# Kernel optimization log

Hardware: AMD Instinct MI355X
Metric: run time of the kernel (lower is better)

## Reference

```python
import jax, jax.numpy as jnp
import numpy as np

POOL = (2, 2)
B, H, W, C = 8, 128, 128, 256
FLAT_OUT = (H * POOL[0]) * (W * POOL[1]) * C  # 16,777,216


def setup_inputs() -> dict:
    key = jax.random.key(0)
    k1, k2 = jax.random.split(key)
    updates = jax.random.normal(k1, (B, H, W, C), dtype=jnp.float32)
    mask = jax.random.randint(k2, (B, H, W, C), 0, FLAT_OUT, dtype=jnp.int32)
    return {"updates": updates, "mask": mask}


def reference(updates, mask):
    ph, pw = POOL
    b, h, w, c = updates.shape
    hout, wout = h * ph, w * pw
    flat_input_size = h * w * c            # NOTE: original uses INPUT size as batch offset
    flat_output_size = hout * wout * c
    # per-batch offset (replicates b * flat_input_size from the TF code)
    batch_range = jnp.arange(b, dtype=jnp.int32).reshape(-1, 1, 1, 1)
    flat_mask = (mask.astype(jnp.int32) + batch_range * flat_input_size).reshape(-1)
    flat_updates = updates.reshape(-1)
    flat_output = jnp.zeros((b * flat_output_size,), dtype=updates.dtype)
    flat_output = flat_output.at[flat_mask].add(flat_updates)
    return flat_output.reshape(b, hout, wout, c)
```

## Files before the change

### kernel.cpp

```cpp
#include <hip/hip_runtime.h>


typedef float floatx4 __attribute__((ext_vector_type(4)));

constexpr int FLAT_IN   = 1 << 22;
constexpr int N_ELEMS   = 8 * FLAT_IN;
constexpr int OUT_WIN   = 7 * FLAT_IN + (1 << 24);
constexpr int OUT_TOTAL = 134217728;
constexpr int BKT_SHIFT = 14;
constexpr int BKT_SIZE  = 1 << BKT_SHIFT;
constexpr int NB        = OUT_WIN >> BKT_SHIFT;
constexpr int PBLOCK    = 1024;
constexpr int CHUNK     = 131072;
constexpr int NBLK      = N_ELEMS / CHUNK;
constexpr int ITERS     = CHUNK / (4 * PBLOCK);
constexpr int SEGS      = 8;
constexpr int SEG_ROWS  = NBLK / SEGS;

constexpr size_t WS_PAIRS  = 0;
constexpr size_t WS_HIST   = 268435456;
constexpr size_t WS_SEGSUM = WS_HIST + (size_t)NBLK * NB * 4;
constexpr size_t WS_BBASE  = WS_SEGSUM + (size_t)SEGS * NB * 4;
constexpr size_t WS_NEEDED = WS_BBASE + (size_t)(NB + 1) * 4;

__global__ __launch_bounds__(256) void zero_kernel(floatx4* __restrict__ p, int n4) {
  int i = blockIdx.x * 256 + threadIdx.x;
  int stride = gridDim.x * 256;
  floatx4 z = {0.f, 0.f, 0.f, 0.f};
  for (; i < n4; i += stride) __builtin_nontemporal_store(z, p + i);
}

__global__ __launch_bounds__(PBLOCK) void p1_hist(const int4* __restrict__ mask4,
                                                  int* __restrict__ hist) {
  __shared__ int cnt[NB];
  const int blk = blockIdx.x, tid = threadIdx.x;
  for (int j = tid; j < NB; j += PBLOCK) cnt[j] = 0;
  __syncthreads();
  const int base4 = blk * (CHUNK / 4);
  const int boff = (blk * CHUNK) & ~(FLAT_IN - 1);
  #pragma unroll 4
  for (int k = 0; k < ITERS; ++k) {
    int4 m = mask4[base4 + k * PBLOCK + tid];
    atomicAdd(&cnt[(m.x + boff) >> BKT_SHIFT], 1);
    atomicAdd(&cnt[(m.y + boff) >> BKT_SHIFT], 1);
    atomicAdd(&cnt[(m.z + boff) >> BKT_SHIFT], 1);
    atomicAdd(&cnt[(m.w + boff) >> BKT_SHIFT], 1);
  }
  __syncthreads();
  for (int j = tid; j < NB; j += PBLOCK) hist[blk * NB + j] = cnt[j];
}

__global__ __launch_bounds__(256) void p2_segsum(const int* __restrict__ hist,
                                                 int* __restrict__ segsum) {
  int b = blockIdx.x * 256 + threadIdx.x;
  int seg = blockIdx.y;
  const int* p = hist + (size_t)(seg * SEG_ROWS) * NB + b;
  int s = 0;
  #pragma unroll 4
  for (int k = 0; k < SEG_ROWS; ++k) s += p[(size_t)k * NB];
  segsum[seg * NB + b] = s;
}

__global__ __launch_bounds__(256) void p2_scan(const int* __restrict__ segsum,
                                               int* __restrict__ bbase) {
  __shared__ int tot[NB];
  __shared__ int partial[256];
  const int t = threadIdx.x;
  for (int j = t; j < NB; j += 256) {
    int s = 0;
    #pragma unroll
    for (int g = 0; g < SEGS; ++g) s += segsum[g * NB + j];
    tot[j] = s;
  }
  __syncthreads();
  int local = 0;
  #pragma unroll
  for (int k = 0; k < NB / 256; ++k) local += tot[t * (NB / 256) + k];
  partial[t] = local;
  __syncthreads();
  for (int off = 1; off < 256; off <<= 1) {
    int tmp = (t >= off) ? partial[t - off] : 0;
    __syncthreads();
    partial[t] += tmp;
    __syncthreads();
  }
  int run = partial[t] - local;
  #pragma unroll
  for (int k = 0; k < NB / 256; ++k) {
    int b = t * (NB / 256) + k;
    bbase[b] = run;
    run += tot[b];
  }
  if (t == 255) bbase[NB] = run;
}

__global__ __launch_bounds__(256) void p2_expand(int* __restrict__ hist,
                                                 const int* __restrict__ segsum) {
  int b = blockIdx.x * 256 + threadIdx.x;
  int seg = blockIdx.y;
  int run = 0;
  for (int g = 0; g < seg; ++g) run += segsum[g * NB + b];
  int* p = hist + (size_t)(seg * SEG_ROWS) * NB + b;
  for (int k = 0; k < SEG_ROWS; ++k) {
    int v = p[(size_t)k * NB];
    p[(size_t)k * NB] = run;
    run += v;
  }
}

__global__ __launch_bounds__(PBLOCK) void p3_place(const int4* __restrict__ mask4,
                                                   const float4* __restrict__ upd4,
                                                   const int* __restrict__ hist,
                                                   const int* __restrict__ bbase,
                                                   int2* __restrict__ pairs) {
  __shared__ int cnt[NB];
  __shared__ int rowbase[NB];
  const int blk = blockIdx.x, tid = threadIdx.x;
  for (int j = tid; j < NB; j += PBLOCK) {
    cnt[j] = 0;
    rowbase[j] = bbase[j] + hist[blk * NB + j];
  }
  __syncthreads();
  const int base4 = blk * (CHUNK / 4);
  const int boff = (blk * CHUNK) & ~(FLAT_IN - 1);
  #pragma unroll 2
  for (int k = 0; k < ITERS; ++k) {
    int j4 = base4 + k * PBLOCK + tid;
    int4 m = mask4[j4];
    float4 u = upd4[j4];
    {
      int idx = m.x + boff; int b = idx >> BKT_SHIFT;
      int r = atomicAdd(&cnt[b], 1);
      pairs[rowbase[b] + r] = make_int2(idx, __float_as_int(u.x));
    }
    {
      int idx = m.y + boff; int b = idx >> BKT_SHIFT;
      int r = atomicAdd(&cnt[b], 1);
      pairs[rowbase[b] + r] = make_int2(idx, __float_as_int(u.y));
    }
    {
      int idx = m.z + boff; int b = idx >> BKT_SHIFT;
      int r = atomicAdd(&cnt[b], 1);
      pairs[rowbase[b] + r] = make_int2(idx, __float_as_int(u.z));
    }
    {
      int idx = m.w + boff; int b = idx >> BKT_SHIFT;
      int r = atomicAdd(&cnt[b], 1);
      pairs[rowbase[b] + r] = make_int2(idx, __float_as_int(u.w));
    }
  }
}

__global__ __launch_bounds__(256) void p4_apply(const int2* __restrict__ pairs,
                                                const int* __restrict__ bbase,
                                                float* __restrict__ out) {
  __shared__ float win[BKT_SIZE];
  const int bkt = blockIdx.x, tid = threadIdx.x;
  floatx4* w4 = (floatx4*)win;
  floatx4 z = {0.f, 0.f, 0.f, 0.f};
  #pragma unroll
  for (int k = 0; k < BKT_SIZE / 1024; ++k) w4[k * 256 + tid] = z;
  __syncthreads();
  const int s = bbase[bkt], e = bbase[bkt + 1];
  const int s4 = (s + 1) & ~1;
  if ((s & 1) && s < e && tid == 0) {
    int2 p = pairs[s];
    atomicAdd(&win[p.x & (BKT_SIZE - 1)], __int_as_float(p.y));
  }
  const int n2 = (e > s4) ? ((e - s4) >> 1) : 0;
  const int4* pv = (const int4*)(pairs + s4);
  for (int i = tid; i < n2; i += 256) {
    int4 q = pv[i];
    atomicAdd(&win[q.x & (BKT_SIZE - 1)], __int_as_float(q.y));
    atomicAdd(&win[q.z & (BKT_SIZE - 1)], __int_as_float(q.w));
  }
  if ((e > s4) && ((e - s4) & 1) && tid == 0) {
    int2 p = pairs[e - 1];
    atomicAdd(&win[p.x & (BKT_SIZE - 1)], __int_as_float(p.y));
  }
  __syncthreads();
  floatx4* o4 = (floatx4*)(out + (size_t)bkt * BKT_SIZE);
  #pragma unroll
  for (int k = 0; k < BKT_SIZE / 1024; ++k)
    __builtin_nontemporal_store(w4[k * 256 + tid], o4 + k * 256 + tid);
}

__global__ __launch_bounds__(256) void scatter_add4_kernel(
    const float4* __restrict__ upd4, const int4* __restrict__ msk4,
    float* __restrict__ out, int n4) {
  int j = blockIdx.x * blockDim.x + threadIdx.x;
  if (j >= n4) return;
  float4 u = upd4[j];
  int4 m = msk4[j];
  int base = (j * 4) & ~(FLAT_IN - 1);
  unsafeAtomicAdd(out + (base + m.x), u.x);
  unsafeAtomicAdd(out + (base + m.y), u.y);
  unsafeAtomicAdd(out + (base + m.z), u.z);
  unsafeAtomicAdd(out + (base + m.w), u.w);
}

extern "C" void kernel_launch(void* const* d_in, const int* in_sizes, int n_in,
                              void* d_out, int out_size, void* d_ws, size_t ws_size,
                              hipStream_t stream) {
  const float* updates = (const float*)d_in[0];
  const int*   mask    = (const int*)d_in[1];
  float*       out     = (float*)d_out;
  const int n = in_sizes[0];

  const bool fast = (n == N_ELEMS) && (out_size == OUT_TOTAL) && (ws_size >= WS_NEEDED);

  if (!fast) {
    int n4z = out_size / 4;
    zero_kernel<<<(n4z + 2047) / 2048, 256, 0, stream>>>((floatx4*)d_out, n4z);
    int n4 = n / 4;
    scatter_add4_kernel<<<(n4 + 255) / 256, 256, 0, stream>>>(
        (const float4*)updates, (const int4*)mask, out, n4);
    return;
  }

  char* ws = (char*)d_ws;
  int2* pairs  = (int2*)(ws + WS_PAIRS);
  int*  hist   = (int*)(ws + WS_HIST);
  int*  segsum = (int*)(ws + WS_SEGSUM);
  int*  bbase  = (int*)(ws + WS_BBASE);

  {
    int n4 = (OUT_TOTAL - OUT_WIN) / 4;
    zero_kernel<<<5376, 256, 0, stream>>>((floatx4*)(out + OUT_WIN), n4);
  }
  p1_hist<<<NBLK, PBLOCK, 0, stream>>>((const int4*)mask, hist);
  p2_segsum<<<dim3(NB / 256, SEGS), 256, 0, stream>>>(hist, segsum);
  p2_scan<<<1, 256, 0, stream>>>(segsum, bbase);
  p2_expand<<<dim3(NB / 256, SEGS), 256, 0, stream>>>(hist, segsum);
  p3_place<<<NBLK, PBLOCK, 0, stream>>>((const int4*)mask, (const float4*)updates,
                                        hist, bbase, pairs);
  p4_apply<<<NB, 256, 0, stream>>>(pairs, bbase, out);
}
```

Before: 1.212 ms.

## Split bucket sort into coarse and fine passes with wave-aggregated fine placement

Replaces the single-pass bucket sort over 16K-element buckets with two passes. A coarse pass places pairs into 64K-element buckets using a small per-block shared histogram, with pairs staged in the unused tail of the output buffer. A fine pass then splits each coarse bucket into four fine buckets, using ballot-based wave aggregation to cut shared atomics. This is meant to shrink the per-block histogram and scan work and make the scattered pair writes more local, at the cost of an extra full read and write of the pair array.

```diff
diff --git a/kernel.cpp b/kernel.cpp
--- a/kernel.cpp
+++ b/kernel.cpp
@@ -7,21 +7,28 @@
 constexpr int N_ELEMS   = 8 * FLAT_IN;
 constexpr int OUT_WIN   = 7 * FLAT_IN + (1 << 24);
 constexpr int OUT_TOTAL = 134217728;
-constexpr int BKT_SHIFT = 14;
-constexpr int BKT_SIZE  = 1 << BKT_SHIFT;
-constexpr int NB        = OUT_WIN >> BKT_SHIFT;
-constexpr int PBLOCK    = 1024;
-constexpr int CHUNK     = 131072;
-constexpr int NBLK      = N_ELEMS / CHUNK;
-constexpr int ITERS     = CHUNK / (4 * PBLOCK);
-constexpr int SEGS      = 8;
-constexpr int SEG_ROWS  = NBLK / SEGS;
+
+constexpr int FB_SHIFT = 14;
+constexpr int BKT_SIZE = 1 << FB_SHIFT;
+constexpr int NBF      = OUT_WIN >> FB_SHIFT;
+constexpr int CB_SHIFT = 16;
+constexpr int NBC      = OUT_WIN >> CB_SHIFT;
+constexpr int NBC_PAD  = 768;
+
+constexpr int PBLOCK   = 1024;
+constexpr int CHUNK    = 131072;
+constexpr int NBLK     = N_ELEMS / CHUNK;
+constexpr int ITERS    = CHUNK / (4 * PBLOCK);
+constexpr int SEGS     = 8;
+constexpr int SEG_ROWS = NBLK / SEGS;
 
 constexpr size_t WS_PAIRS  = 0;
-constexpr size_t WS_HIST   = 268435456;
-constexpr size_t WS_SEGSUM = WS_HIST + (size_t)NBLK * NB * 4;
-constexpr size_t WS_BBASE  = WS_SEGSUM + (size_t)SEGS * NB * 4;
-constexpr size_t WS_NEEDED = WS_BBASE + (size_t)(NB + 1) * 4;
+constexpr size_t WS_HISTC  = 268435456;
+constexpr size_t WS_SEGC   = WS_HISTC + (size_t)NBLK * NBC_PAD * 4;
+constexpr size_t WS_BBC    = WS_SEGC + (size_t)SEGS * NBC_PAD * 4;
+constexpr size_t WS_FH     = WS_BBC + 3328;
+constexpr size_t WS_BBF    = WS_FH + (size_t)NBF * 4;
+constexpr size_t WS_NEEDED = WS_BBF + (size_t)(NBF + 1) * 4;
 
 __global__ __launch_bounds__(256) void zero_kernel(floatx4* __restrict__ p, int n4) {
   int i = blockIdx.x * 256 + threadIdx.x;
@@ -31,51 +38,62 @@
 }
 
 __global__ __launch_bounds__(PBLOCK) void p1_hist(const int4* __restrict__ mask4,
-                                                  int* __restrict__ hist) {
-  __shared__ int cnt[NB];
+                                                  int* __restrict__ hist_c,
+                                                  int* __restrict__ fhist) {
+  __shared__ int cnt[1024];
   const int blk = blockIdx.x, tid = threadIdx.x;
-  for (int j = tid; j < NB; j += PBLOCK) cnt[j] = 0;
+  if (tid < 1024) cnt[tid] = 0;
   __syncthreads();
   const int base4 = blk * (CHUNK / 4);
-  const int boff = (blk * CHUNK) & ~(FLAT_IN - 1);
   #pragma unroll 4
   for (int k = 0; k < ITERS; ++k) {
     int4 m = mask4[base4 + k * PBLOCK + tid];
-    atomicAdd(&cnt[(m.x + boff) >> BKT_SHIFT], 1);
-    atomicAdd(&cnt[(m.y + boff) >> BKT_SHIFT], 1);
-    atomicAdd(&cnt[(m.z + boff) >> BKT_SHIFT], 1);
-    atomicAdd(&cnt[(m.w + boff) >> BKT_SHIFT], 1);
-  }
-  __syncthreads();
-  for (int j = tid; j < NB; j += PBLOCK) hist[blk * NB + j] = cnt[j];
+    atomicAdd(&cnt[m.x >> FB_SHIFT], 1);
+    atomicAdd(&cnt[m.y >> FB_SHIFT], 1);
+    atomicAdd(&cnt[m.z >> FB_SHIFT], 1);
+    atomicAdd(&cnt[m.w >> FB_SHIFT], 1);
+  }
+  __syncthreads();
+  const int boff = (blk * CHUNK) & ~(FLAT_IN - 1);
+  const int f0   = boff >> FB_SHIFT;
+  const int cb0  = f0 >> 2;
+  for (int j = tid; j < 1024; j += PBLOCK)
+    if (cnt[j]) atomicAdd(&fhist[f0 + j], cnt[j]);
+  for (int j = tid; j < NBC_PAD; j += PBLOCK) {
+    int v = 0;
+    int jj = j - cb0;
+    if (jj >= 0 && jj < 256)
+      v = cnt[4 * jj] + cnt[4 * jj + 1] + cnt[4 * jj + 2] + cnt[4 * jj + 3];
+    hist_c[blk * NBC_PAD + j] = v;
+  }
 }
 
 __global__ __launch_bounds__(256) void p2_segsum(const int* __restrict__ hist,
                                                  int* __restrict__ segsum) {
   int b = blockIdx.x * 256 + threadIdx.x;
   int seg = blockIdx.y;
-  const int* p = hist + (size_t)(seg * SEG_ROWS) * NB + b;
+  const int* p = hist + (size_t)(seg * SEG_ROWS) * NBC_PAD + b;
   int s = 0;
   #pragma unroll 4
-  for (int k = 0; k < SEG_ROWS; ++k) s += p[(size_t)k * NB];
-  segsum[seg * NB + b] = s;
-}
-
-__global__ __launch_bounds__(256) void p2_scan(const int* __restrict__ segsum,
-                                               int* __restrict__ bbase) {
-  __shared__ int tot[NB];
+  for (int k = 0; k < SEG_ROWS; ++k) s += p[(size_t)k * NBC_PAD];
+  segsum[seg * NBC_PAD + b] = s;
+}
+
+__global__ __launch_bounds__(256) void p2_scan_c(const int* __restrict__ segsum,
+                                                 int* __restrict__ bbase) {
+  __shared__ int tot[NBC_PAD];
   __shared__ int partial[256];
   const int t = threadIdx.x;
-  for (int j = t; j < NB; j += 256) {
+  for (int j = t; j < NBC_PAD; j += 256) {
     int s = 0;
     #pragma unroll
-    for (int g = 0; g < SEGS; ++g) s += segsum[g * NB + j];
+    for (int g = 0; g < SEGS; ++g) s += segsum[g * NBC_PAD + j];
     tot[j] = s;
   }
   __syncthreads();
   int local = 0;
   #pragma unroll
-  for (int k = 0; k < NB / 256; ++k) local += tot[t * (NB / 256) + k];
+  for (int k = 0; k < NBC_PAD / 256; ++k) local += tot[t * (NBC_PAD / 256) + k];
   partial[t] = local;
   __syncthreads();
   for (int off = 1; off < 256; off <<= 1) {
@@ -86,12 +104,12 @@
   }
   int run = partial[t] - local;
   #pragma unroll
-  for (int k = 0; k < NB / 256; ++k) {
-    int b = t * (NB / 256) + k;
+  for (int k = 0; k < NBC_PAD / 256; ++k) {
+    int b = t * (NBC_PAD / 256) + k;
     bbase[b] = run;
     run += tot[b];
   }
-  if (t == 255) bbase[NB] = run;
+  if (t == 255) bbase[NBC_PAD] = run;
 }
 
 __global__ __launch_bounds__(256) void p2_expand(int* __restrict__ hist,
@@ -99,55 +117,131 @@
   int b = blockIdx.x * 256 + threadIdx.x;
   int seg = blockIdx.y;
   int run = 0;
-  for (int g = 0; g < seg; ++g) run += segsum[g * NB + b];
-  int* p = hist + (size_t)(seg * SEG_ROWS) * NB + b;
+  for (int g = 0; g < seg; ++g) run += segsum[g * NBC_PAD + b];
+  int* p = hist + (size_t)(seg * SEG_ROWS) * NBC_PAD + b;
   for (int k = 0; k < SEG_ROWS; ++k) {
-    int v = p[(size_t)k * NB];
-    p[(size_t)k * NB] = run;
+    int v = p[(size_t)k * NBC_PAD];
+    p[(size_t)k * NBC_PAD] = run;
     run += v;
   }
 }
 
-__global__ __launch_bounds__(PBLOCK) void p3_place(const int4* __restrict__ mask4,
-                                                   const float4* __restrict__ upd4,
-                                                   const int* __restrict__ hist,
-                                                   const int* __restrict__ bbase,
-                                                   int2* __restrict__ pairs) {
-  __shared__ int cnt[NB];
-  __shared__ int rowbase[NB];
+__global__ __launch_bounds__(256) void p2_scan_f(const int* __restrict__ fhist,
+                                                 int* __restrict__ bbase) {
+  __shared__ int tot[NBF];
+  __shared__ int partial[256];
+  const int t = threadIdx.x;
+  for (int j = t; j < NBF; j += 256) tot[j] = fhist[j];
+  __syncthreads();
+  int local = 0;
+  #pragma unroll
+  for (int k = 0; k < NBF / 256; ++k) local += tot[t * (NBF / 256) + k];
+  partial[t] = local;
+  __syncthreads();
+  for (int off = 1; off < 256; off <<= 1) {
+    int tmp = (t >= off) ? partial[t - off] : 0;
+    __syncthreads();
+    partial[t] += tmp;
+    __syncthreads();
+  }
+  int run = partial[t] - local;
+  #pragma unroll
+  for (int k = 0; k < NBF / 256; ++k) {
+    int b = t * (NBF / 256) + k;
+    bbase[b] = run;
+    run += tot[b];
+  }
+  if (t == 255) bbase[NBF] = run;
+}
+
+__global__ __launch_bounds__(PBLOCK) void p3a_place(const int4* __restrict__ mask4,
+                                                    const float4* __restrict__ upd4,
+                                                    const int* __restrict__ hist_c,
+                                                    const int* __restrict__ bbase_c,
+                                                    int2* __restrict__ pout) {
+  __shared__ int cnt[256];
+  __shared__ int rowbase[256];
   const int blk = blockIdx.x, tid = threadIdx.x;
-  for (int j = tid; j < NB; j += PBLOCK) {
-    cnt[j] = 0;
-    rowbase[j] = bbase[j] + hist[blk * NB + j];
+  const int boff = (blk * CHUNK) & ~(FLAT_IN - 1);
+  const int cb0 = boff >> CB_SHIFT;
+  if (tid < 256) {
+    cnt[tid] = 0;
+    rowbase[tid] = bbase_c[cb0 + tid] + hist_c[blk * NBC_PAD + cb0 + tid];
   }
   __syncthreads();
   const int base4 = blk * (CHUNK / 4);
-  const int boff = (blk * CHUNK) & ~(FLAT_IN - 1);
   #pragma unroll 2
   for (int k = 0; k < ITERS; ++k) {
     int j4 = base4 + k * PBLOCK + tid;
     int4 m = mask4[j4];
     float4 u = upd4[j4];
     {
-      int idx = m.x + boff; int b = idx >> BKT_SHIFT;
-      int r = atomicAdd(&cnt[b], 1);
-      pairs[rowbase[b] + r] = make_int2(idx, __float_as_int(u.x));
+      int b = m.x >> CB_SHIFT; int r = atomicAdd(&cnt[b], 1);
+      pout[rowbase[b] + r] = make_int2(m.x + boff, __float_as_int(u.x));
     }
     {
-      int idx = m.y + boff; int b = idx >> BKT_SHIFT;
-      int r = atomicAdd(&cnt[b], 1);
-      pairs[rowbase[b] + r] = make_int2(idx, __float_as_int(u.y));
+      int b = m.y >> CB_SHIFT; int r = atomicAdd(&cnt[b], 1);
+      pout[rowbase[b] + r] = make_int2(m.y + boff, __float_as_int(u.y));
     }
     {
-      int idx = m.z + boff; int b = idx >> BKT_SHIFT;
-      int r = atomicAdd(&cnt[b], 1);
-      pairs[rowbase[b] + r] = make_int2(idx, __float_as_int(u.z));
+      int b = m.z >> CB_SHIFT; int r = atomicAdd(&cnt[b], 1);
+      pout[rowbase[b] + r] = make_int2(m.z + boff, __float_as_int(u.z));
     }
     {
-      int idx = m.w + boff; int b = idx >> BKT_SHIFT;
-      int r = atomicAdd(&cnt[b], 1);
-      pairs[rowbase[b] + r] = make_int2(idx, __float_as_int(u.w));
+      int b = m.w >> CB_SHIFT; int r = atomicAdd(&cnt[b], 1);
+      pout[rowbase[b] + r] = make_int2(m.w + boff, __float_as_int(u.w));
     }
+  }
+}
+
+__device__ __forceinline__ void pushA(int idx, int val, int* cnt, const int* fb,
+                                      int2* __restrict__ pout) {
+  int f = (idx >> FB_SHIFT) & 3;
+  unsigned long long act = __ballot(1);
+  unsigned long long b0 = __ballot(f & 1);
+  unsigned long long b1 = __ballot(f & 2);
+  unsigned long long mf = ((f & 1) ? b0 : ~b0) & ((f & 2) ? b1 : ~b1) & act;
+  int lane = threadIdx.x & 63;
+  int rank = __popcll(mf & ((1ull << lane) - 1ull));
+  int leader = __ffsll((unsigned long long)mf) - 1;
+  int r0 = 0;
+  if (lane == leader) r0 = atomicAdd(&cnt[f], __popcll(mf));
+  r0 = __shfl(r0, leader);
+  pout[fb[f] + r0 + rank] = make_int2(idx, val);
+}
+
+__global__ __launch_bounds__(512) void p3b_fine(const int2* __restrict__ pin,
+                                                const int* __restrict__ bbase_c,
+                                                const int* __restrict__ bbase_f,
+                                                int2* __restrict__ pout) {
+  __shared__ int cnt[4];
+  __shared__ int fb[4];
+  const int cb = blockIdx.x, tid = threadIdx.x;
+  if (tid < 4) {
+    cnt[tid] = 0;
+    fb[tid] = bbase_f[cb * 4 + tid];
+  }
+  __syncthreads();
+  const int s = bbase_c[cb], e = bbase_c[cb + 1];
+  const int s4 = (s + 1) & ~1;
+  if ((s & 1) && s < e && tid == 0) {
+    int2 p = pin[s];
+    int f = (p.x >> FB_SHIFT) & 3;
+    int r = atomicAdd(&cnt[f], 1);
+    pout[fb[f] + r] = p;
+  }
+  const int n2 = (e > s4) ? ((e - s4) >> 1) : 0;
+  const int4* pv = (const int4*)(pin + s4);
+  for (int i = tid; i < n2; i += 512) {
+    int4 q = pv[i];
+    pushA(q.x, q.y, cnt, fb, pout);
+    pushA(q.z, q.w, cnt, fb, pout);
+  }
+  if ((e > s4) && ((e - s4) & 1) && tid == 0) {
+    int2 p = pin[e - 1];
+    int f = (p.x >> FB_SHIFT) & 3;
+    int r = atomicAdd(&cnt[f], 1);
+    pout[fb[f] + r] = p;
   }
 }
 
@@ -219,20 +313,26 @@
   }
 
   char* ws = (char*)d_ws;
-  int2* pairs  = (int2*)(ws + WS_PAIRS);
-  int*  hist   = (int*)(ws + WS_HIST);
-  int*  segsum = (int*)(ws + WS_SEGSUM);
-  int*  bbase  = (int*)(ws + WS_BBASE);
-
+  int2* pairs_f = (int2*)(ws + WS_PAIRS);
+  int*  hist_c  = (int*)(ws + WS_HISTC);
+  int*  segsum  = (int*)(ws + WS_SEGC);
+  int*  bbase_c = (int*)(ws + WS_BBC);
+  int*  fhist   = (int*)(ws + WS_FH);
+  int*  bbase_f = (int*)(ws + WS_BBF);
+  int2* pairs_c = (int2*)(out + OUT_WIN);
+
+  zero_kernel<<<1, 256, 0, stream>>>((floatx4*)fhist, NBF / 4);
+  p1_hist<<<NBLK, PBLOCK, 0, stream>>>((const int4*)mask, hist_c, fhist);
+  p2_segsum<<<dim3(NBC_PAD / 256, SEGS), 256, 0, stream>>>(hist_c, segsum);
+  p2_scan_c<<<1, 256, 0, stream>>>(segsum, bbase_c);
+  p2_expand<<<dim3(NBC_PAD / 256, SEGS), 256, 0, stream>>>(hist_c, segsum);
+  p2_scan_f<<<1, 256, 0, stream>>>(fhist, bbase_f);
+  p3a_place<<<NBLK, PBLOCK, 0, stream>>>((const int4*)mask, (const float4*)updates,
+                                         hist_c, bbase_c, pairs_c);
+  p3b_fine<<<NBC, 512, 0, stream>>>(pairs_c, bbase_c, bbase_f, pairs_f);
   {
     int n4 = (OUT_TOTAL - OUT_WIN) / 4;
     zero_kernel<<<5376, 256, 0, stream>>>((floatx4*)(out + OUT_WIN), n4);
   }
-  p1_hist<<<NBLK, PBLOCK, 0, stream>>>((const int4*)mask, hist);
-  p2_segsum<<<dim3(NB / 256, SEGS), 256, 0, stream>>>(hist, segsum);
-  p2_scan<<<1, 256, 0, stream>>>(segsum, bbase);
-  p2_expand<<<dim3(NB / 256, SEGS), 256, 0, stream>>>(hist, segsum);
-  p3_place<<<NBLK, PBLOCK, 0, stream>>>((const int4*)mask, (const float4*)updates,
-                                        hist, bbase, pairs);
-  p4_apply<<<NB, 256, 0, stream>>>(pairs, bbase, out);
-}
+  p4_apply<<<NBF, 256, 0, stream>>>(pairs_f, bbase_f, out);
+}
```

Measured after the change: 1.219 ms. About the same (+0.6%).
